# Optimization experiments

Measured on AMD Instinct MI355X. Metric: run time of the kernel, lower is better.

The kernel has to match this reference:

```python
import jax, jax.numpy as jnp
import numpy as np

D = 512      # model_channels
H = 4        # heads
L = 4        # num_transfomers_layers
DK = D // H
EPS = 1e-5


def inorm(x):
    # nn.InstanceNorm1d(d_model) applied to (bs, seq, d_model): normalizes over
    # the last (d_model) axis per token, no affine params.
    m = jnp.mean(x, axis=-1, keepdims=True)
    v = jnp.var(x, axis=-1, keepdims=True)
    return (x - m) * jax.lax.rsqrt(v + EPS)


def mha(xq, xkv, w, b, mask):
    # w: [4, D, D] (q,k,v,out), b: [4, D]; mask: [bs,S,S] (1 = masked)
    bs, S, _ = xq.shape
    q = (xq @ w[0] + b[0]).reshape(bs, S, H, DK).transpose(0, 2, 1, 3)
    k = (xkv @ w[1] + b[1]).reshape(bs, S, H, DK).transpose(0, 2, 1, 3)
    v = (xkv @ w[2] + b[2]).reshape(bs, S, H, DK).transpose(0, 2, 1, 3)
    scores = jnp.einsum('bhqd,bhkd->bhqk', q, k) / jnp.sqrt(jnp.float32(DK))
    scores = jnp.where(mask[:, None] == 1, jnp.float32(-1e9), scores)
    attn = jax.nn.softmax(scores, axis=-1)
    out = jnp.einsum('bhqk,bhkd->bhqd', attn, v)
    out = out.transpose(0, 2, 1, 3).reshape(bs, S, D)
    return out @ w[3] + b[3]


def setup_inputs() -> dict:
    key = jax.random.key(0)
    ks = jax.random.split(key, 24)
    bs, S = 16, 512
    sc = 0.02
    inp = {
        'x': jax.random.normal(ks[0], (bs, S, 18), jnp.float32),
        'cond': jax.random.normal(ks[1], (bs, S, 89), jnp.float32),
        'door_mask': jax.random.randint(ks[2], (bs, S, S), 0, 2, jnp.int32),
        'self_mask': jax.random.randint(ks[3], (bs, S, S), 0, 2, jnp.int32),
        'gen_mask': jax.random.randint(ks[4], (bs, S, S), 0, 2, jnp.int32),
        # attention params: [L, 3 branches (door,self,gen), 4 projs (q,k,v,out)]
        'attn_w': jax.random.normal(ks[5], (L, 3, 4, D, D), jnp.float32) * sc,
        'attn_b': jnp.zeros((L, 3, 4, D), jnp.float32),
        'ff_w1': jax.random.normal(ks[6], (L, D, 2 * D), jnp.float32) * sc,
        'ff_b1': jnp.zeros((L, 2 * D), jnp.float32),
        'ff_w2': jax.random.normal(ks[7], (L, 2 * D, D), jnp.float32) * sc,
        'ff_b2': jnp.zeros((L, D), jnp.float32),
        'in_w': jax.random.normal(ks[8], (18, D), jnp.float32) * sc,
        'in_b': jnp.zeros((D,), jnp.float32),
        'cond_w': jax.random.normal(ks[9], (89, D), jnp.float32) * sc,
        'cond_b': jnp.zeros((D,), jnp.float32),
        'out1_w': jax.random.normal(ks[10], (D, D), jnp.float32) * sc,
        'out1_b': jnp.zeros((D,), jnp.float32),
        'out2_w': jax.random.normal(ks[11], (D, D // 2), jnp.float32) * sc,
        'out2_b': jnp.zeros((D // 2,), jnp.float32),
        'out3_w': jax.random.normal(ks[12], (D // 2, 2), jnp.float32) * sc,
        'out3_b': jnp.zeros((2,), jnp.float32),
    }
    return inp


def reference(x, cond, door_mask, self_mask, gen_mask,
              attn_w, attn_b, ff_w1, ff_b1, ff_w2, ff_b2,
              in_w, in_b, cond_w, cond_b,
              out1_w, out1_b, out2_w, out2_b, out3_w, out3_b):
    h = (x @ in_w + in_b) + (cond @ cond_w + cond_b)  # [bs,S,D]
    for l in range(L):
        h2 = inorm(h)
        h = (h
             + mha(h2, h2, attn_w[l, 0], attn_b[l, 0], door_mask)
             + mha(h2, h2, attn_w[l, 1], attn_b[l, 1], self_mask)
             + mha(h2, h2, attn_w[l, 2], attn_b[l, 2], gen_mask))
        h2 = inorm(h)
        h = h + jax.nn.relu(h2 @ ff_w1[l] + ff_b1[l]) @ ff_w2[l] + ff_b2[l]
    out = jax.nn.relu(h @ out1_w + out1_b)
    out = jax.nn.relu(out @ out2_w + out2_b)
    out = out @ out3_w + out3_b  # [bs,S,2]
    return out
```

## Files before the change

kernel.cpp:

```cpp
#include <hip/hip_runtime.h>
#include <hip/hip_bf16.h>

#define DEV static __device__ __forceinline__

typedef __attribute__((ext_vector_type(8))) short bfx8;
typedef __attribute__((ext_vector_type(4))) float f32x4;
typedef __attribute__((ext_vector_type(4))) unsigned short us4;

DEV unsigned short f2bf(float f){
  unsigned u = __builtin_bit_cast(unsigned, f);
  u += 0x7fffu + ((u >> 16) & 1u);
  return (unsigned short)(u >> 16);
}
DEV float bf2f(unsigned short h){
  unsigned u = ((unsigned)h) << 16;
  return __builtin_bit_cast(float, u);
}
DEV void gld16(const void* g, void* l){
  __builtin_amdgcn_global_load_lds((const __attribute__((address_space(1))) void*)g,
                                   (__attribute__((address_space(3))) void*)l, 16, 0, 0);
}
DEV f32x4 mfma16(bfx8 a, bfx8 b, f32x4 c){
  return __builtin_amdgcn_mfma_f32_16x16x32_bf16(a, b, c, 0, 0, 0);
}

__global__ __launch_bounds__(256, 2)
void wconv_kernel(const float* __restrict__ attn_w, const float* __restrict__ ff_w1,
                  const float* __restrict__ ff_w2, const float* __restrict__ out1_w,
                  const float* __restrict__ out2_w,
                  unsigned short* __restrict__ bqkv, unsigned short* __restrict__ bout,
                  unsigned short* __restrict__ bff1, unsigned short* __restrict__ bff2,
                  unsigned short* __restrict__ bo1, unsigned short* __restrict__ bo2)
{
  __shared__ float ts[64][65];
  const int z = blockIdx.z;
  const float* src; unsigned short* dst; int K, N, stride;
  if (z < 48){
    int l = z / 12, br = (z % 12) >> 2, p = z & 3;
    src = attn_w + (size_t)z * 262144; K = 512; N = 512;
    if (p < 3){ dst = bqkv + (size_t)l * 4608 * 512 + (size_t)(br * 3 + p) * 262144; stride = 512; }
    else      { dst = bout + (size_t)l * 512 * 1536 + (size_t)br * 512;              stride = 1536; }
  } else if (z < 52){
    int l = z - 48; src = ff_w1 + (size_t)l * 524288; K = 512; N = 1024;
    dst = bff1 + (size_t)l * 524288; stride = 512;
  } else if (z < 56){
    int l = z - 52; src = ff_w2 + (size_t)l * 524288; K = 1024; N = 512;
    dst = bff2 + (size_t)l * 524288; stride = 1024;
  } else if (z == 56){
    src = out1_w; K = 512; N = 512; dst = bo1; stride = 512;
  } else {
    src = out2_w; K = 512; N = 256; dst = bo2; stride = 512;
  }
  const int n0 = blockIdx.x << 6, k0 = blockIdx.y << 6;
  if (n0 >= N || k0 >= K) return;
  const int tx = threadIdx.x & 63, ty = threadIdx.x >> 6;
  #pragma unroll
  for (int i = 0; i < 16; ++i){
    int row = (ty << 4) + i;
    ts[row][tx] = src[(size_t)(k0 + row) * N + n0 + tx];
  }
  __syncthreads();
  #pragma unroll
  for (int i = 0; i < 16; ++i){
    int row = (ty << 4) + i;
    dst[(size_t)(n0 + row) * stride + k0 + tx] = f2bf(ts[tx][row]);
  }
}

__global__ __launch_bounds__(256, 4)
void mpack_kernel(const int* __restrict__ m0, const int* __restrict__ m1,
                  const int* __restrict__ m2, unsigned long long* __restrict__ mp)
{
  const int row = (blockIdx.x << 2) + (threadIdx.x >> 6);
  const int lane = threadIdx.x & 63;
  const int* src = (row < 8192) ? (m0 + (size_t)row * 512)
                 : (row < 16384 ? (m1 + (size_t)(row - 8192) * 512)
                                : (m2 + (size_t)(row - 16384) * 512));
  #pragma unroll
  for (int c = 0; c < 8; ++c){
    const int v = src[(c << 6) + lane];
    const unsigned long long b = __ballot(v != 0);
    if (lane == c) mp[(size_t)row * 8 + c] = b;
  }
}

__global__ __launch_bounds__(256, 4)
void embed_kernel(const float* __restrict__ x, const float* __restrict__ cond,
                  const float* __restrict__ in_w, const float* __restrict__ in_b,
                  const float* __restrict__ cond_w, const float* __restrict__ cond_b,
                  float* __restrict__ h)
{
  __shared__ float xs[18];
  __shared__ float cs[89];
  const int m = blockIdx.x;
  const int tid = threadIdx.x;
  if (tid < 18) xs[tid] = x[(size_t)m * 18 + tid];
  if (tid >= 32 && tid < 121) cs[tid - 32] = cond[(size_t)m * 89 + (tid - 32)];
  __syncthreads();
  #pragma unroll
  for (int hf = 0; hf < 2; ++hf){
    const int c = tid + (hf << 8);
    float a = in_b[c] + cond_b[c];
    #pragma unroll
    for (int k = 0; k < 18; ++k) a += xs[k] * in_w[k * 512 + c];
    for (int k = 0; k < 89; ++k) a += cs[k] * cond_w[k * 512 + c];
    h[(size_t)m * 512 + c] = a;
  }
}

__global__ __launch_bounds__(256, 4)
void inorm_kernel(const float* __restrict__ in, unsigned short* __restrict__ ob)
{
  const int wid = (blockIdx.x << 2) + (threadIdx.x >> 6);
  const int lane = threadIdx.x & 63;
  const float* row = in + (size_t)wid * 512;
  const float4 v0 = *(const float4*)(row + (lane << 2));
  const float4 v1 = *(const float4*)(row + 256 + (lane << 2));
  float s = v0.x + v0.y + v0.z + v0.w + v1.x + v1.y + v1.z + v1.w;
  float q = v0.x*v0.x + v0.y*v0.y + v0.z*v0.z + v0.w*v0.w
          + v1.x*v1.x + v1.y*v1.y + v1.z*v1.z + v1.w*v1.w;
  #pragma unroll
  for (int sh = 1; sh < 64; sh <<= 1){
    s += __shfl_xor(s, sh, 64);
    q += __shfl_xor(q, sh, 64);
  }
  const float mean = s * (1.f / 512.f);
  const float var = q * (1.f / 512.f) - mean * mean;
  const float rs = rsqrtf(var + 1e-5f);
  us4 o0, o1;
  o0[0] = f2bf((v0.x - mean) * rs); o0[1] = f2bf((v0.y - mean) * rs);
  o0[2] = f2bf((v0.z - mean) * rs); o0[3] = f2bf((v0.w - mean) * rs);
  o1[0] = f2bf((v1.x - mean) * rs); o1[1] = f2bf((v1.y - mean) * rs);
  o1[2] = f2bf((v1.z - mean) * rs); o1[3] = f2bf((v1.w - mean) * rs);
  *(us4*)(ob + (size_t)wid * 512 + (lane << 2)) = o0;
  *(us4*)(ob + (size_t)wid * 512 + 256 + (lane << 2)) = o1;
}

__global__ void f2b_kernel(const float* __restrict__ in, unsigned short* __restrict__ ob, int n)
{
  const int i = (blockIdx.x * 256 + threadIdx.x) << 2;
  if (i >= n) return;
  const float4 v = *(const float4*)(in + i);
  us4 o; o[0] = f2bf(v.x); o[1] = f2bf(v.y); o[2] = f2bf(v.z); o[3] = f2bf(v.w);
  *(us4*)(ob + i) = o;
}

template<int MODE>
__global__ __launch_bounds__(256, 2)
void gemm_bt(const unsigned short* __restrict__ A, const unsigned short* __restrict__ B,
             const float* __restrict__ bias, float* __restrict__ Cf,
             unsigned short* __restrict__ Cb, unsigned short* __restrict__ qkp,
             unsigned short* __restrict__ vtp, int M, int N, int K)
{
  __shared__ unsigned short As[128 * 64];
  __shared__ unsigned short Bs[128 * 64];
  const int tid = threadIdx.x;
  const int w = tid >> 6, lane = tid & 63;
  const int wm = w >> 1, wn = w & 1;
  const int lr = lane & 15, lh = lane >> 4;
  const int m0 = blockIdx.x << 7, n0 = blockIdx.y << 7;
  const int rA = lane >> 3;
  const int cA = (lane & 7) << 3;

  f32x4 acc[4][4];
  #pragma unroll
  for (int i = 0; i < 4; ++i)
    #pragma unroll
    for (int j = 0; j < 4; ++j) acc[i][j] = (f32x4)0.f;

  const int nkt = K >> 6;
  auto stage = [&](int kt){
    #pragma unroll
    for (int c = 0; c < 4; ++c){
      const int r = (c << 5) + (w << 3) + rA;
      gld16(A + (size_t)(m0 + r) * K + (kt << 6) + cA,
            (char*)As + ((c << 5) + (w << 3)) * 128);
      gld16(B + (size_t)(n0 + r) * K + (kt << 6) + cA,
            (char*)Bs + ((c << 5) + (w << 3)) * 128);
    }
  };
  stage(0);
  for (int kt = 0; kt < nkt; ++kt){
    __syncthreads();
    #pragma unroll
    for (int kk = 0; kk < 2; ++kk){
      bfx8 af[4], bg[4];
      #pragma unroll
      for (int i = 0; i < 4; ++i)
        af[i] = *(const bfx8*)(As + ((wm << 6) + (i << 4) + lr) * 64 + (kk << 5) + (lh << 3));
      #pragma unroll
      for (int j = 0; j < 4; ++j)
        bg[j] = *(const bfx8*)(Bs + ((wn << 6) + (j << 4) + lr) * 64 + (kk << 5) + (lh << 3));
      #pragma unroll
      for (int i = 0; i < 4; ++i)
        #pragma unroll
        for (int j = 0; j < 4; ++j)
          acc[i][j] = mfma16(af[i], bg[j], acc[i][j]);
    }
    __syncthreads();
    if (kt + 1 < nkt) stage(kt + 1);
  }
  #pragma unroll
  for (int i = 0; i < 4; ++i){
    const int row = m0 + (wm << 6) + (i << 4) + (lh << 2);
    #pragma unroll
    for (int j = 0; j < 4; ++j){
      const int col = n0 + (wn << 6) + (j << 4) + lr;
      if constexpr (MODE == 1){
        const float bv = bias ? bias[col] : 0.f;
        #pragma unroll
        for (int r = 0; r < 4; ++r){
          float v = acc[i][j][r] + bv;
          v = fmaxf(v, 0.f);
          Cb[(size_t)(row + r) * N + col] = f2bf(v);
        }
      } else if constexpr (MODE == 2){
        const float bv = bias ? bias[col] : 0.f;
        #pragma unroll
        for (int r = 0; r < 4; ++r){
          const size_t idx = (size_t)(row + r) * N + col;
          Cf[idx] += acc[i][j][r] + bv;
        }
      } else {
        const int br = col / 1536;
        const int rem = col - br * 1536;
        const int p = rem >> 9;
        const int c = rem & 511;
        const float bv = bias ? bias[(size_t)((br << 2) + p) * 512 + c] : 0.f;
        if (p < 2){
          #pragma unroll
          for (int r = 0; r < 4; ++r)
            qkp[((size_t)((br << 1) + p) * 8192 + row + r) * 512 + c] = f2bf(acc[i][j][r] + bv);
        } else {
          const int b_ = row >> 9, s0 = row & 511;
          const int hi = c >> 7, dk = c & 127;
          us4 pk;
          #pragma unroll
          for (int r = 0; r < 4; ++r) pk[r] = f2bf(acc[i][j][r] + bv);
          *(us4*)(vtp + (((size_t)(br * 16 + b_) * 4 + hi) * 128 + dk) * 512 + s0) = pk;
        }
      }
    }
  }
}

__global__ __launch_bounds__(256, 2)
void attn_kernel(const unsigned short* __restrict__ qk, const unsigned short* __restrict__ vt,
                 const unsigned* __restrict__ mp, unsigned short* __restrict__ outp)
{
  __shared__ unsigned short KV[2][4096];
  __shared__ unsigned short Pl[4][16 * 40];
  __shared__ unsigned Mk[64 * 17];
  const int tid = threadIdx.x;
  const int w = tid >> 6, lane = tid & 63;
  const int lr = lane & 15, lh = lane >> 4;
  const int id = blockIdx.x;
  const int pair = (id & 7) * 192 / 8 + ((id >> 3) >> 3);
  const int qt = (id >> 3) & 7;
  const int br = pair >> 6, bh = pair & 63;
  const int b = bh >> 2, h = bh & 3;
  const int q0 = (qt << 6) + (w << 4);

  const unsigned short* qbase = qk + ((size_t)(br * 2 + 0) * 8192 + (size_t)b * 512) * 512 + h * 128;
  const unsigned short* kbase = qk + ((size_t)(br * 2 + 1) * 8192 + (size_t)b * 512) * 512 + h * 128;
  const unsigned short* vbase = vt + ((size_t)(br * 16 + b) * 4 + h) * 128 * 512;
  const unsigned* mrow = mp + ((size_t)br * 8192 + (size_t)b * 512 + (qt << 6)) * 16;

  for (int idx = tid; idx < 1024; idx += 256){
    const int rw = idx >> 4, wd = idx & 15;
    Mk[rw * 17 + wd] = mrow[rw * 16 + wd];
  }

  bfx8 aq[4];
  #pragma unroll
  for (int t = 0; t < 4; ++t)
    aq[t] = *(const bfx8*)(qbase + (size_t)(q0 + lr) * 512 + (t << 5) + (lh << 3));

  f32x4 sc[16][2];
  const float scale = 0.08838834764831845f;

  auto stageK = [&](int kt){
    char* dst = (char*)KV[kt & 1];
    #pragma unroll
    for (int c2 = 0; c2 < 2; ++c2){
      const int trow = (c2 << 4) + (w << 2) + (lane >> 4);
      const int g = (lane & 15) ^ (trow & 7);
      gld16(kbase + (size_t)((kt << 5) + trow) * 512 + (g << 3),
            dst + ((c2 << 4) + (w << 2)) * 256);
    }
  };
  auto stageV = [&](int kt){
    char* dst = (char*)KV[kt & 1];
    #pragma unroll
    for (int c2 = 0; c2 < 2; ++c2){
      const int drow = (c2 << 6) + (w << 4) + (lane >> 2);
      const int g = (lane & 3) ^ (drow & 3);
      gld16(vbase + (size_t)drow * 512 + (kt << 5) + (g << 3),
            dst + ((c2 << 6) + (w << 4)) * 64);
    }
  };

  stageK(0);
  for (int kt = 0; kt < 16; ++kt){
    __syncthreads();
    if (kt < 15) stageK(kt + 1);
    const unsigned short* Ksb = KV[kt & 1];
    #pragma unroll
    for (int j = 0; j < 2; ++j){
      const int rk = (j << 4) + lr;
      f32x4 a2 = (f32x4)0.f;
      #pragma unroll
      for (int t = 0; t < 4; ++t){
        const int s = ((t << 2) + lh) ^ (rk & 7);
        bfx8 bk = *(const bfx8*)(Ksb + rk * 128 + (s << 3));
        a2 = mfma16(aq[t], bk, a2);
      }
      #pragma unroll
      for (int r = 0; r < 4; ++r){
        const int qloc = (w << 4) + (lh << 2) + r;
        const unsigned mword = Mk[qloc * 17 + kt];
        const int bit = (mword >> ((j << 4) + lr)) & 1;
        sc[kt][j][r] = bit ? -1e9f : a2[r] * scale;
      }
    }
  }

  float mx[4] = {-3e38f, -3e38f, -3e38f, -3e38f};
  #pragma unroll
  for (int kt = 0; kt < 16; ++kt)
    #pragma unroll
    for (int j = 0; j < 2; ++j)
      #pragma unroll
      for (int r = 0; r < 4; ++r) mx[r] = fmaxf(mx[r], sc[kt][j][r]);
  #pragma unroll
  for (int s = 1; s < 16; s <<= 1)
    #pragma unroll
    for (int r = 0; r < 4; ++r) mx[r] = fmaxf(mx[r], __shfl_xor(mx[r], s, 64));
  float sm[4] = {0.f, 0.f, 0.f, 0.f};
  #pragma unroll
  for (int kt = 0; kt < 16; ++kt)
    #pragma unroll
    for (int j = 0; j < 2; ++j)
      #pragma unroll
      for (int r = 0; r < 4; ++r){
        const float pv = __expf(sc[kt][j][r] - mx[r]);
        sc[kt][j][r] = pv;
        sm[r] += pv;
      }
  #pragma unroll
  for (int s = 1; s < 16; s <<= 1)
    #pragma unroll
    for (int r = 0; r < 4; ++r) sm[r] += __shfl_xor(sm[r], s, 64);
  float linv[4];
  #pragma unroll
  for (int r = 0; r < 4; ++r) linv[r] = 1.f / sm[r];

  f32x4 ao[8];
  #pragma unroll
  for (int j = 0; j < 8; ++j) ao[j] = (f32x4)0.f;
  unsigned short* pw = Pl[w];
  __syncthreads();
  stageV(0);
  for (int kt = 0; kt < 16; ++kt){
    __syncthreads();
    if (kt < 15) stageV(kt + 1);
    #pragma unroll
    for (int j = 0; j < 2; ++j)
      #pragma unroll
      for (int r = 0; r < 4; ++r)
        pw[((lh << 2) + r) * 40 + (j << 4) + lr] = f2bf(sc[kt][j][r] * linv[r]);
    bfx8 pa = *(const bfx8*)(pw + lr * 40 + (lh << 3));
    const unsigned short* Vsb = KV[kt & 1];
    #pragma unroll
    for (int j = 0; j < 8; ++j){
      const int dd = (j << 4) + lr;
      const int s = lh ^ (dd & 3);
      bfx8 bv = *(const bfx8*)(Vsb + dd * 32 + (s << 3));
      ao[j] = mfma16(pa, bv, ao[j]);
    }
  }
  const size_t obase = (size_t)(b * 512) * 1536 + br * 512 + h * 128;
  #pragma unroll
  for (int j = 0; j < 8; ++j){
    const int d = (j << 4) + lr;
    #pragma unroll
    for (int r = 0; r < 4; ++r){
      const int q = q0 + (lh << 2) + r;
      outp[obase + (size_t)q * 1536 + d] = f2bf(ao[j][r]);
    }
  }
}

__global__ __launch_bounds__(256, 4)
void out3_kernel(const unsigned short* __restrict__ t2, const float* __restrict__ w,
                 const float* __restrict__ b2, float* __restrict__ outp)
{
  const int row = (blockIdx.x << 2) + (threadIdx.x >> 6);
  const int lane = threadIdx.x & 63;
  const unsigned short* rp = t2 + (size_t)row * 256 + (lane << 2);
  float a0 = 0.f, a1 = 0.f;
  #pragma unroll
  for (int k = 0; k < 4; ++k){
    const float v = bf2f(rp[k]);
    const int kk = (lane << 2) + k;
    a0 += v * w[kk * 2 + 0];
    a1 += v * w[kk * 2 + 1];
  }
  #pragma unroll
  for (int s = 1; s < 64; s <<= 1){
    a0 += __shfl_xor(a0, s, 64);
    a1 += __shfl_xor(a1, s, 64);
  }
  if (lane == 0){
    outp[(size_t)row * 2 + 0] = a0 + b2[0];
    outp[(size_t)row * 2 + 1] = a1 + b2[1];
  }
}

extern "C" void kernel_launch(void* const* d_in, const int* in_sizes, int n_in,
                              void* d_out, int out_size, void* d_ws, size_t ws_size,
                              hipStream_t stream)
{
  const float* x      = (const float*)d_in[0];
  const float* cond   = (const float*)d_in[1];
  const int*   mdoor  = (const int*)d_in[2];
  const int*   mself  = (const int*)d_in[3];
  const int*   mgen   = (const int*)d_in[4];
  const float* attn_w = (const float*)d_in[5];
  const float* attn_b = (const float*)d_in[6];
  const float* ff_w1  = (const float*)d_in[7];
  const float* ff_b1  = (const float*)d_in[8];
  const float* ff_w2  = (const float*)d_in[9];
  const float* ff_b2  = (const float*)d_in[10];
  const float* in_w   = (const float*)d_in[11];
  const float* in_b   = (const float*)d_in[12];
  const float* cond_w = (const float*)d_in[13];
  const float* cond_b = (const float*)d_in[14];
  const float* out1_w = (const float*)d_in[15];
  const float* out1_b = (const float*)d_in[16];
  const float* out2_w = (const float*)d_in[17];
  const float* out2_b = (const float*)d_in[18];
  const float* out3_w = (const float*)d_in[19];
  const float* out3_b = (const float*)d_in[20];

  char* p = (char*)d_ws;
  auto carve = [&](size_t bytes) -> char* {
    char* r = p; p += (bytes + 255) & ~(size_t)255; return r;
  };
  float*          h    = (float*)carve(8192ull * 512 * 4);
  unsigned short* h2   = (unsigned short*)carve(8192ull * 512 * 2);
  unsigned short* bqkv = (unsigned short*)carve(4ull * 4608 * 512 * 2);
  unsigned short* bout = (unsigned short*)carve(4ull * 512 * 1536 * 2);
  unsigned short* bff1 = (unsigned short*)carve(4ull * 1024 * 512 * 2);
  unsigned short* bff2 = (unsigned short*)carve(4ull * 512 * 1024 * 2);
  unsigned short* bo1  = (unsigned short*)carve(512ull * 512 * 2);
  unsigned short* bo2  = (unsigned short*)carve(256ull * 512 * 2);
  unsigned short* qkb  = (unsigned short*)carve(6ull * 8192 * 512 * 2);
  unsigned short* vtb  = (unsigned short*)carve(3ull * 16 * 4 * 128 * 512 * 2);
  unsigned short* att  = (unsigned short*)carve(8192ull * 1536 * 2);
  unsigned short* t    = (unsigned short*)carve(8192ull * 1024 * 2);
  unsigned short* t2   = (unsigned short*)carve(8192ull * 256 * 2);
  unsigned long long* mpk = (unsigned long long*)carve(24576ull * 8 * 8);
  float* outf = (float*)d_out;

  wconv_kernel<<<dim3(16, 16, 58), 256, 0, stream>>>(attn_w, ff_w1, ff_w2, out1_w, out2_w,
                                                     bqkv, bout, bff1, bff2, bo1, bo2);
  mpack_kernel<<<dim3(6144), 256, 0, stream>>>(mdoor, mself, mgen, mpk);
  embed_kernel<<<dim3(8192), 256, 0, stream>>>(x, cond, in_w, in_b, cond_w, cond_b, h);
  for (int l = 0; l < 4; ++l){
    inorm_kernel<<<dim3(2048), 256, 0, stream>>>(h, h2);
    gemm_bt<3><<<dim3(64, 36), 256, 0, stream>>>(h2, bqkv + (size_t)l * 4608 * 512,
        attn_b + (size_t)l * 6144, nullptr, nullptr, qkb, vtb, 8192, 4608, 512);
    attn_kernel<<<dim3(1536), 256, 0, stream>>>(qkb, vtb, (const unsigned*)mpk, att);
    gemm_bt<2><<<dim3(64, 4), 256, 0, stream>>>(att, bout + (size_t)l * 512 * 1536,
        nullptr, h, nullptr, nullptr, nullptr, 8192, 512, 1536);
    inorm_kernel<<<dim3(2048), 256, 0, stream>>>(h, h2);
    gemm_bt<1><<<dim3(64, 8), 256, 0, stream>>>(h2, bff1 + (size_t)l * 1024 * 512,
        ff_b1 + (size_t)l * 1024, nullptr, t, nullptr, nullptr, 8192, 1024, 512);
    gemm_bt<2><<<dim3(64, 4), 256, 0, stream>>>(t, bff2 + (size_t)l * 512 * 1024,
        ff_b2 + (size_t)l * 512, h, nullptr, nullptr, nullptr, 8192, 512, 1024);
  }
  f2b_kernel<<<dim3(4096), 256, 0, stream>>>(h, h2, 8192 * 512);
  gemm_bt<1><<<dim3(64, 4), 256, 0, stream>>>(h2, bo1, out1_b, nullptr, att, nullptr, nullptr, 8192, 512, 512);
  gemm_bt<1><<<dim3(64, 2), 256, 0, stream>>>(att, bo2, out2_b, nullptr, t2, nullptr, nullptr, 8192, 256, 512);
  out3_kernel<<<dim3(2048), 256, 0, stream>>>(t2, out3_w, out3_b, outf);
}
```

Baseline: 1.298 ms.

## Add 256x256 pipelined GEMM, direct-global attention loads, batched embed rows

Adds a new 512-thread GEMM with 256x256 output tiles. It uses a double-buffered LDS pipeline with explicit vmcnt waits, raw barriers, an XOR swizzle and a block-id remap, and replaces most of the 128x128 GEMM launches with it. The attention kernel drops LDS staging of K and V, reads them straight from global memory, loads masks per wave, and raises wave priority around the MFMAs. The embed kernel now handles 8 rows per block so each weight load is reused. The larger tiles give few blocks for the N=512 GEMMs (64 blocks), which risks underusing the GPU, and uncached global K/V reads may cost bandwidth.

```diff
diff --git a/kernel.cpp b/kernel.cpp
--- a/kernel.cpp
+++ b/kernel.cpp
@@ -23,6 +23,9 @@
 DEV f32x4 mfma16(bfx8 a, bfx8 b, f32x4 c){
   return __builtin_amdgcn_mfma_f32_16x16x32_bf16(a, b, c, 0, 0, 0);
 }
+
+#define BAR() do{ asm volatile("" ::: "memory"); __builtin_amdgcn_s_barrier(); \
+                  asm volatile("" ::: "memory"); }while(0)
 
 __global__ __launch_bounds__(256, 2)
 void wconv_kernel(const float* __restrict__ attn_w, const float* __restrict__ ff_w1,
@@ -90,21 +93,33 @@
                   const float* __restrict__ cond_w, const float* __restrict__ cond_b,
                   float* __restrict__ h)
 {
-  __shared__ float xs[18];
-  __shared__ float cs[89];
-  const int m = blockIdx.x;
+  __shared__ float xs[8][18];
+  __shared__ float cs[8][89];
+  const int m0 = blockIdx.x << 3;
   const int tid = threadIdx.x;
-  if (tid < 18) xs[tid] = x[(size_t)m * 18 + tid];
-  if (tid >= 32 && tid < 121) cs[tid - 32] = cond[(size_t)m * 89 + (tid - 32)];
+  for (int i = tid; i < 144; i += 256) xs[i / 18][i % 18] = x[(size_t)m0 * 18 + i];
+  for (int i = tid; i < 712; i += 256) cs[i / 89][i % 89] = cond[(size_t)m0 * 89 + i];
   __syncthreads();
   #pragma unroll
   for (int hf = 0; hf < 2; ++hf){
     const int c = tid + (hf << 8);
-    float a = in_b[c] + cond_b[c];
-    #pragma unroll
-    for (int k = 0; k < 18; ++k) a += xs[k] * in_w[k * 512 + c];
-    for (int k = 0; k < 89; ++k) a += cs[k] * cond_w[k * 512 + c];
-    h[(size_t)m * 512 + c] = a;
+    const float bsum = in_b[c] + cond_b[c];
+    float a[8];
+    #pragma unroll
+    for (int mi = 0; mi < 8; ++mi) a[mi] = bsum;
+    #pragma unroll
+    for (int k = 0; k < 18; ++k){
+      const float wv = in_w[k * 512 + c];
+      #pragma unroll
+      for (int mi = 0; mi < 8; ++mi) a[mi] += xs[mi][k] * wv;
+    }
+    for (int k = 0; k < 89; ++k){
+      const float wv = cond_w[k * 512 + c];
+      #pragma unroll
+      for (int mi = 0; mi < 8; ++mi) a[mi] += cs[mi][k] * wv;
+    }
+    #pragma unroll
+    for (int mi = 0; mi < 8; ++mi) h[(size_t)(m0 + mi) * 512 + c] = a[mi];
   }
 }
 
@@ -149,8 +164,7 @@
 __global__ __launch_bounds__(256, 2)
 void gemm_bt(const unsigned short* __restrict__ A, const unsigned short* __restrict__ B,
              const float* __restrict__ bias, float* __restrict__ Cf,
-             unsigned short* __restrict__ Cb, unsigned short* __restrict__ qkp,
-             unsigned short* __restrict__ vtp, int M, int N, int K)
+             unsigned short* __restrict__ Cb, int M, int N, int K)
 {
   __shared__ unsigned short As[128 * 64];
   __shared__ unsigned short Bs[128 * 64];
@@ -206,21 +220,148 @@
     #pragma unroll
     for (int j = 0; j < 4; ++j){
       const int col = n0 + (wn << 6) + (j << 4) + lr;
+      const float bv = bias ? bias[col] : 0.f;
+      #pragma unroll
+      for (int r = 0; r < 4; ++r){
+        float v = acc[i][j][r] + bv;
+        if constexpr (MODE == 1){
+          v = fmaxf(v, 0.f);
+          Cb[(size_t)(row + r) * N + col] = f2bf(v);
+        } else {
+          Cf[(size_t)(row + r) * N + col] += v;
+        }
+      }
+    }
+  }
+}
+
+template<int MODE>
+__global__ __launch_bounds__(512, 2)
+void gemm256(const unsigned short* __restrict__ A, const unsigned short* __restrict__ B,
+             const float* __restrict__ bias, float* __restrict__ Cf,
+             unsigned short* __restrict__ Cb, unsigned short* __restrict__ qkp,
+             unsigned short* __restrict__ vtp, int M, int N, int K)
+{
+  __shared__ unsigned short L[2][2][2][8192];
+  const int tid = threadIdx.x;
+  const int w = tid >> 6, lane = tid & 63;
+  const int wr = w >> 2, wc = w & 3;
+  const int lr = lane & 15, lh = lane >> 4;
+
+  const int nwg = gridDim.x;
+  const int id = blockIdx.x;
+  const int wg = (id & 7) * (nwg >> 3) + (id >> 3);
+  const int mt = wg & 31, nt = wg >> 5;
+  const int m0 = mt << 8, n0 = nt << 8;
+
+  f32x4 acc[8][4];
+  #pragma unroll
+  for (int f = 0; f < 8; ++f)
+    #pragma unroll
+    for (int n = 0; n < 4; ++n) acc[f][n] = (f32x4)0.f;
+
+  auto stage_half = [&](int buf, int kt, int kh, int mat){
+    const unsigned short* G = mat ? B : A;
+    const int base0 = mat ? n0 : m0;
+    const int r0 = (w << 4) + (lane >> 2);
+    const int ga = (lane & 3) ^ ((r0 >> 1) & 3);
+    gld16(G + (size_t)(base0 + r0) * K + kt * 64 + kh * 32 + ga * 8,
+          &L[buf][mat][kh][(w << 4) * 32]);
+    gld16(G + (size_t)(base0 + 128 + r0) * K + kt * 64 + kh * 32 + ga * 8,
+          &L[buf][mat][kh][(128 + (w << 4)) * 32]);
+  };
+
+  bfx8 af[8];
+  auto loadA = [&](int buf, int kh){
+    #pragma unroll
+    for (int f = 0; f < 8; ++f){
+      const int ra = wr * 128 + f * 16 + lr;
+      af[f] = *(const bfx8*)&L[buf][0][kh][ra * 32 + ((lh ^ ((ra >> 1) & 3)) << 3)];
+    }
+  };
+  auto ldB1 = [&](int buf, int kh, int g) -> bfx8 {
+    const int rb = wc * 64 + g * 16 + lr;
+    return *(const bfx8*)&L[buf][1][kh][rb * 32 + ((lh ^ ((rb >> 1) & 3)) << 3)];
+  };
+  auto mmaN = [&](int n, bfx8 b){
+    __builtin_amdgcn_s_setprio(1);
+    #pragma unroll
+    for (int f = 0; f < 8; ++f) acc[f][n] = mfma16(af[f], b, acc[f][n]);
+    __builtin_amdgcn_s_setprio(0);
+  };
+
+  const int nkt = K >> 6;
+  const int niter = nkt >> 1;
+
+  stage_half(0, 0, 0, 0); stage_half(0, 0, 0, 1);
+  stage_half(0, 0, 1, 0); stage_half(0, 0, 1, 1);
+  stage_half(1, 1, 0, 0); stage_half(1, 1, 0, 1);
+  stage_half(1, 1, 1, 0);
+
+  for (int i = 0; i < niter; ++i){
+    const int t0 = 2 * i;
+    const bool pre = (i + 1 < niter);
+    bfx8 b0, b1;
+    asm volatile("s_waitcnt vmcnt(6)" ::: "memory");
+    BAR();
+    stage_half(1, t0 + 1, 1, 1);
+    loadA(0, 0);
+    b0 = ldB1(0, 0, 0); b1 = ldB1(0, 0, 1);
+    mmaN(0, b0); mmaN(1, b1);
+    BAR();
+    if (pre) stage_half(0, t0 + 2, 0, 0);
+    b0 = ldB1(0, 0, 2); b1 = ldB1(0, 0, 3);
+    mmaN(2, b0); mmaN(3, b1);
+    BAR();
+    if (pre) stage_half(0, t0 + 2, 0, 1);
+    loadA(0, 1);
+    b0 = ldB1(0, 1, 0); b1 = ldB1(0, 1, 1);
+    mmaN(0, b0); mmaN(1, b1);
+    BAR();
+    if (pre) stage_half(0, t0 + 2, 1, 0);
+    b0 = ldB1(0, 1, 2); b1 = ldB1(0, 1, 3);
+    mmaN(2, b0); mmaN(3, b1);
+    if (pre) asm volatile("s_waitcnt vmcnt(6)" ::: "memory");
+    else     asm volatile("s_waitcnt vmcnt(0)" ::: "memory");
+    BAR();
+    if (pre) stage_half(0, t0 + 2, 1, 1);
+    loadA(1, 0);
+    b0 = ldB1(1, 0, 0); b1 = ldB1(1, 0, 1);
+    mmaN(0, b0); mmaN(1, b1);
+    BAR();
+    if (pre) stage_half(1, t0 + 3, 0, 0);
+    b0 = ldB1(1, 0, 2); b1 = ldB1(1, 0, 3);
+    mmaN(2, b0); mmaN(3, b1);
+    BAR();
+    if (pre) stage_half(1, t0 + 3, 0, 1);
+    loadA(1, 1);
+    b0 = ldB1(1, 1, 0); b1 = ldB1(1, 1, 1);
+    mmaN(0, b0); mmaN(1, b1);
+    BAR();
+    if (pre) stage_half(1, t0 + 3, 1, 0);
+    b0 = ldB1(1, 1, 2); b1 = ldB1(1, 1, 3);
+    mmaN(2, b0); mmaN(3, b1);
+  }
+
+  #pragma unroll
+  for (int f = 0; f < 8; ++f){
+    const int row = m0 + wr * 128 + f * 16 + (lh << 2);
+    #pragma unroll
+    for (int n = 0; n < 4; ++n){
+      const int col = n0 + wc * 64 + n * 16 + lr;
       if constexpr (MODE == 1){
         const float bv = bias ? bias[col] : 0.f;
         #pragma unroll
         for (int r = 0; r < 4; ++r){
-          float v = acc[i][j][r] + bv;
+          float v = acc[f][n][r] + bv;
           v = fmaxf(v, 0.f);
           Cb[(size_t)(row + r) * N + col] = f2bf(v);
         }
       } else if constexpr (MODE == 2){
         const float bv = bias ? bias[col] : 0.f;
         #pragma unroll
-        for (int r = 0; r < 4; ++r){
-          const size_t idx = (size_t)(row + r) * N + col;
-          Cf[idx] += acc[i][j][r] + bv;
-        }
+        for (int r = 0; r < 4; ++r)
+          Cf[(size_t)(row + r) * N + col] += acc[f][n][r] + bv;
       } else {
         const int br = col / 1536;
         const int rem = col - br * 1536;
@@ -230,13 +371,13 @@
         if (p < 2){
           #pragma unroll
           for (int r = 0; r < 4; ++r)
-            qkp[((size_t)((br << 1) + p) * 8192 + row + r) * 512 + c] = f2bf(acc[i][j][r] + bv);
+            qkp[((size_t)((br << 1) + p) * 8192 + row + r) * 512 + c] = f2bf(acc[f][n][r] + bv);
         } else {
           const int b_ = row >> 9, s0 = row & 511;
           const int hi = c >> 7, dk = c & 127;
           us4 pk;
           #pragma unroll
-          for (int r = 0; r < 4; ++r) pk[r] = f2bf(acc[i][j][r] + bv);
+          for (int r = 0; r < 4; ++r) pk[r] = f2bf(acc[f][n][r] + bv);
           *(us4*)(vtp + (((size_t)(br * 16 + b_) * 4 + hi) * 128 + dk) * 512 + s0) = pk;
         }
       }
@@ -248,14 +389,13 @@
 void attn_kernel(const unsigned short* __restrict__ qk, const unsigned short* __restrict__ vt,
                  const unsigned* __restrict__ mp, unsigned short* __restrict__ outp)
 {
-  __shared__ unsigned short KV[2][4096];
   __shared__ unsigned short Pl[4][16 * 40];
-  __shared__ unsigned Mk[64 * 17];
+  __shared__ unsigned Mk[4][16 * 17];
   const int tid = threadIdx.x;
   const int w = tid >> 6, lane = tid & 63;
   const int lr = lane & 15, lh = lane >> 4;
   const int id = blockIdx.x;
-  const int pair = (id & 7) * 192 / 8 + ((id >> 3) >> 3);
+  const int pair = (id & 7) * 24 + (id >> 6);
   const int qt = (id >> 3) & 7;
   const int br = pair >> 6, bh = pair & 63;
   const int b = bh >> 2, h = bh & 3;
@@ -264,12 +404,16 @@
   const unsigned short* qbase = qk + ((size_t)(br * 2 + 0) * 8192 + (size_t)b * 512) * 512 + h * 128;
   const unsigned short* kbase = qk + ((size_t)(br * 2 + 1) * 8192 + (size_t)b * 512) * 512 + h * 128;
   const unsigned short* vbase = vt + ((size_t)(br * 16 + b) * 4 + h) * 128 * 512;
-  const unsigned* mrow = mp + ((size_t)br * 8192 + (size_t)b * 512 + (qt << 6)) * 16;
-
-  for (int idx = tid; idx < 1024; idx += 256){
+  const unsigned* mrow = mp + ((size_t)br * 8192 + (size_t)b * 512 + (qt << 6) + (w << 4)) * 16;
+
+  unsigned* mk = Mk[w];
+  #pragma unroll
+  for (int u = 0; u < 4; ++u){
+    const int idx = (lane << 2) + u;
     const int rw = idx >> 4, wd = idx & 15;
-    Mk[rw * 17 + wd] = mrow[rw * 16 + wd];
-  }
+    mk[rw * 17 + wd] = mrow[rw * 16 + wd];
+  }
+  asm volatile("s_waitcnt lgkmcnt(0)" ::: "memory");
 
   bfx8 aq[4];
   #pragma unroll
@@ -279,46 +423,22 @@
   f32x4 sc[16][2];
   const float scale = 0.08838834764831845f;
 
-  auto stageK = [&](int kt){
-    char* dst = (char*)KV[kt & 1];
-    #pragma unroll
-    for (int c2 = 0; c2 < 2; ++c2){
-      const int trow = (c2 << 4) + (w << 2) + (lane >> 4);
-      const int g = (lane & 15) ^ (trow & 7);
-      gld16(kbase + (size_t)((kt << 5) + trow) * 512 + (g << 3),
-            dst + ((c2 << 4) + (w << 2)) * 256);
-    }
-  };
-  auto stageV = [&](int kt){
-    char* dst = (char*)KV[kt & 1];
-    #pragma unroll
-    for (int c2 = 0; c2 < 2; ++c2){
-      const int drow = (c2 << 6) + (w << 4) + (lane >> 2);
-      const int g = (lane & 3) ^ (drow & 3);
-      gld16(vbase + (size_t)drow * 512 + (kt << 5) + (g << 3),
-            dst + ((c2 << 6) + (w << 4)) * 64);
-    }
-  };
-
-  stageK(0);
+  #pragma unroll 4
   for (int kt = 0; kt < 16; ++kt){
-    __syncthreads();
-    if (kt < 15) stageK(kt + 1);
-    const unsigned short* Ksb = KV[kt & 1];
     #pragma unroll
     for (int j = 0; j < 2; ++j){
-      const int rk = (j << 4) + lr;
+      const int rk = (kt << 5) + (j << 4) + lr;
       f32x4 a2 = (f32x4)0.f;
+      __builtin_amdgcn_s_setprio(1);
       #pragma unroll
       for (int t = 0; t < 4; ++t){
-        const int s = ((t << 2) + lh) ^ (rk & 7);
-        bfx8 bk = *(const bfx8*)(Ksb + rk * 128 + (s << 3));
+        bfx8 bk = *(const bfx8*)(kbase + (size_t)rk * 512 + (t << 5) + (lh << 3));
         a2 = mfma16(aq[t], bk, a2);
       }
+      __builtin_amdgcn_s_setprio(0);
       #pragma unroll
       for (int r = 0; r < 4; ++r){
-        const int qloc = (w << 4) + (lh << 2) + r;
-        const unsigned mword = Mk[qloc * 17 + kt];
+        const unsigned mword = mk[((lh << 2) + r) * 17 + kt];
         const int bit = (mword >> ((j << 4) + lr)) & 1;
         sc[kt][j][r] = bit ? -1e9f : a2[r] * scale;
       }
@@ -359,25 +479,23 @@
   #pragma unroll
   for (int j = 0; j < 8; ++j) ao[j] = (f32x4)0.f;
   unsigned short* pw = Pl[w];
-  __syncthreads();
-  stageV(0);
+  #pragma unroll 2
   for (int kt = 0; kt < 16; ++kt){
-    __syncthreads();
-    if (kt < 15) stageV(kt + 1);
     #pragma unroll
     for (int j = 0; j < 2; ++j)
       #pragma unroll
       for (int r = 0; r < 4; ++r)
         pw[((lh << 2) + r) * 40 + (j << 4) + lr] = f2bf(sc[kt][j][r] * linv[r]);
+    asm volatile("s_waitcnt lgkmcnt(0)" ::: "memory");
     bfx8 pa = *(const bfx8*)(pw + lr * 40 + (lh << 3));
-    const unsigned short* Vsb = KV[kt & 1];
+    __builtin_amdgcn_s_setprio(1);
     #pragma unroll
     for (int j = 0; j < 8; ++j){
-      const int dd = (j << 4) + lr;
-      const int s = lh ^ (dd & 3);
-      bfx8 bv = *(const bfx8*)(Vsb + dd * 32 + (s << 3));
+      bfx8 bv = *(const bfx8*)(vbase + (size_t)((j << 4) + lr) * 512 + (kt << 5) + (lh << 3));
       ao[j] = mfma16(pa, bv, ao[j]);
     }
+    __builtin_amdgcn_s_setprio(0);
+    asm volatile("" ::: "memory");
   }
   const size_t obase = (size_t)(b * 512) * 1536 + br * 512 + h * 128;
   #pragma unroll
@@ -466,22 +584,22 @@
   wconv_kernel<<<dim3(16, 16, 58), 256, 0, stream>>>(attn_w, ff_w1, ff_w2, out1_w, out2_w,
                                                      bqkv, bout, bff1, bff2, bo1, bo2);
   mpack_kernel<<<dim3(6144), 256, 0, stream>>>(mdoor, mself, mgen, mpk);
-  embed_kernel<<<dim3(8192), 256, 0, stream>>>(x, cond, in_w, in_b, cond_w, cond_b, h);
+  embed_kernel<<<dim3(1024), 256, 0, stream>>>(x, cond, in_w, in_b, cond_w, cond_b, h);
   for (int l = 0; l < 4; ++l){
     inorm_kernel<<<dim3(2048), 256, 0, stream>>>(h, h2);
-    gemm_bt<3><<<dim3(64, 36), 256, 0, stream>>>(h2, bqkv + (size_t)l * 4608 * 512,
+    gemm256<3><<<dim3(576), 512, 0, stream>>>(h2, bqkv + (size_t)l * 4608 * 512,
         attn_b + (size_t)l * 6144, nullptr, nullptr, qkb, vtb, 8192, 4608, 512);
     attn_kernel<<<dim3(1536), 256, 0, stream>>>(qkb, vtb, (const unsigned*)mpk, att);
-    gemm_bt<2><<<dim3(64, 4), 256, 0, stream>>>(att, bout + (size_t)l * 512 * 1536,
+    gemm256<2><<<dim3(64), 512, 0, stream>>>(att, bout + (size_t)l * 512 * 1536,
         nullptr, h, nullptr, nullptr, nullptr, 8192, 512, 1536);
     inorm_kernel<<<dim3(2048), 256, 0, stream>>>(h, h2);
-    gemm_bt<1><<<dim3(64, 8), 256, 0, stream>>>(h2, bff1 + (size_t)l * 1024 * 512,
+    gemm256<1><<<dim3(128), 512, 0, stream>>>(h2, bff1 + (size_t)l * 1024 * 512,
         ff_b1 + (size_t)l * 1024, nullptr, t, nullptr, nullptr, 8192, 1024, 512);
-    gemm_bt<2><<<dim3(64, 4), 256, 0, stream>>>(t, bff2 + (size_t)l * 512 * 1024,
+    gemm256<2><<<dim3(64), 512, 0, stream>>>(t, bff2 + (size_t)l * 512 * 1024,
         ff_b2 + (size_t)l * 512, h, nullptr, nullptr, nullptr, 8192, 512, 1024);
   }
   f2b_kernel<<<dim3(4096), 256, 0, stream>>>(h, h2, 8192 * 512);
-  gemm_bt<1><<<dim3(64, 4), 256, 0, stream>>>(h2, bo1, out1_b, nullptr, att, nullptr, nullptr, 8192, 512, 512);
-  gemm_bt<1><<<dim3(64, 2), 256, 0, stream>>>(att, bo2, out2_b, nullptr, t2, nullptr, nullptr, 8192, 256, 512);
+  gemm256<1><<<dim3(64), 512, 0, stream>>>(h2, bo1, out1_b, nullptr, att, nullptr, nullptr, 8192, 512, 512);
+  gemm_bt<1><<<dim3(64, 2), 256, 0, stream>>>(att, bo2, out2_b, nullptr, t2, 8192, 256, 512);
   out3_kernel<<<dim3(2048), 256, 0, stream>>>(t2, out3_w, out3_b, outf);
 }
```

Measured after the change: 2.599 ms. +100.2%, slower.
